# Optimization experiments

Hardware: AMD Instinct MI355X
Metric: run time of the kernel (lower is better)

Reference implementation:

```python
import jax, jax.numpy as jnp
import numpy as np

B, N, D = 4, 2048, 512
H, DA, DL = 8, 64, 64  # heads, attention_dim, linear_dim
EPS = 1e-6


def _layer_norm(x, eps=EPS):
    # F.layer_norm with no affine params
    mu = jnp.mean(x, axis=-1, keepdims=True)
    var = jnp.var(x, axis=-1, keepdims=True)
    return (x - mu) * jax.lax.rsqrt(var + eps)


def setup_inputs() -> dict:
    key = jax.random.key(0)
    k1, k2, k3, k4 = jax.random.split(key, 4)
    x = jax.random.normal(k1, (B, N, D), dtype=jnp.float32)
    # causal (lower-triangular) valid-attention mask, float {0,1}, shape (B,1,N,N)
    attention_mask = jnp.broadcast_to(
        jnp.tril(jnp.ones((N, N), dtype=jnp.float32))[None, None], (B, 1, N, N)
    )
    # _uvqk: (D, 2*H*DL + 2*H*DA), init normal(0, 0.02)
    uvqk = 0.02 * jax.random.normal(k2, (D, 2 * H * DL + 2 * H * DA), dtype=jnp.float32)
    # _o: Linear(H*DL -> D), xavier uniform
    fan_in, fan_out = H * DL, D
    limit = float(np.sqrt(6.0 / (fan_in + fan_out)))
    o_weight = jax.random.uniform(k3, (fan_out, fan_in), dtype=jnp.float32, minval=-limit, maxval=limit)
    o_bias = jnp.zeros((D,), dtype=jnp.float32)
    return {"x": x, "attention_mask": attention_mask, "uvqk": uvqk,
            "o_weight": o_weight, "o_bias": o_bias}


def reference(x, attention_mask, uvqk, o_weight, o_bias):
    b, n, _ = x.shape
    normed_x = _layer_norm(x)
    mm = jax.nn.silu(normed_x @ uvqk)  # fused uvqk projection + silu
    u, v, q, k = jnp.split(mm, [H * DL, 2 * H * DL, 2 * H * DL + H * DA], axis=-1)
    qh = q.reshape(b, n, H, DA)
    kh = k.reshape(b, n, H, DA)
    vh = v.reshape(b, n, H, DL)
    # silu-activated (non-softmax) attention with mask
    qk = jnp.einsum('bnhd,bmhd->bhnm', qh, kh)
    qk = jax.nn.silu(qk) / n
    qk = qk * attention_mask  # (B,1,N,N) broadcast over heads
    attn = jnp.einsum('bhnm,bmhd->bnhd', qk, vh).reshape(b, n, H * DL)
    # gated norm + output proj + residual
    o_input = u * _layer_norm(attn)
    return o_input @ o_weight.T + o_bias + x
```

## Files before the change

### kernel.cpp

```cpp
#include <hip/hip_runtime.h>

typedef __bf16 bf16x8 __attribute__((ext_vector_type(8)));
typedef float f32x4 __attribute__((ext_vector_type(4)));
typedef float f32x16 __attribute__((ext_vector_type(16)));

__device__ __forceinline__ unsigned short f2bf(float f) {
  return __builtin_bit_cast(unsigned short, (__bf16)f);
}
__device__ __forceinline__ float bfu2f(unsigned short b) {
  unsigned int u = ((unsigned int)b) << 16;
  return __builtin_bit_cast(float, u);
}
__device__ __forceinline__ float silu_f(float x) {
  return x * __builtin_amdgcn_rcpf(1.0f + __expf(-x));
}
__device__ __forceinline__ unsigned pk2(float a, float b) {
  return (unsigned)f2bf(a) | ((unsigned)f2bf(b) << 16);
}

template<int CPR, int NI, int SWZ>
__device__ __forceinline__ void stage16(const __bf16* __restrict__ g, int ld,
                                        __bf16* lds, int wave, int lane) {
#pragma unroll
  for (int t = 0; t < NI; ++t) {
    int cb = (wave * NI + t) * 64;
    int c = cb + lane;
    int row = c / CPR;
    int colb = (c % CPR) ^ (row & SWZ);
    __builtin_amdgcn_global_load_lds(
        (const __attribute__((address_space(1))) unsigned int*)(g + row * ld + colb * 8),
        (__attribute__((address_space(3))) unsigned int*)(lds + cb * 8),
        16, 0, 0);
  }
}


__global__ void k_tr_uvqk(const float* __restrict__ uvqk, __bf16* __restrict__ uvqkT) {
  __shared__ float tile[32][33];
  int n0 = blockIdx.x * 32, k0 = blockIdx.y * 32;
  int tx = threadIdx.x, ty = threadIdx.y;
  for (int i = ty; i < 32; i += 8)
    tile[i][tx] = uvqk[(k0 + i) * 2048 + n0 + tx];
  __syncthreads();
  for (int i = ty; i < 32; i += 8)
    uvqkT[(n0 + i) * 512 + k0 + tx] = (__bf16)tile[tx][i];
}

__global__ void k_prep(const float* __restrict__ x, __bf16* __restrict__ nx,
                       const float* __restrict__ ow, __bf16* __restrict__ owb) {
  int bid = blockIdx.x, t = threadIdx.x;
  if (bid >= 8192) {
    int i = (bid - 8192) * 128 + t;
    float4 v = ((const float4*)ow)[i];
    ushort4 o4;
    o4.x = f2bf(v.x); o4.y = f2bf(v.y); o4.z = f2bf(v.z); o4.w = f2bf(v.w);
    ((ushort4*)owb)[i] = o4;
    return;
  }
  float4 v = ((const float4*)(x + (size_t)bid * 512))[t];
  float s = v.x + v.y + v.z + v.w;
  float ss = v.x * v.x + v.y * v.y + v.z * v.z + v.w * v.w;
#pragma unroll
  for (int o = 32; o > 0; o >>= 1) { s += __shfl_down(s, o); ss += __shfl_down(ss, o); }
  __shared__ float red[4];
  if ((t & 63) == 0) { red[(t >> 6) * 2] = s; red[(t >> 6) * 2 + 1] = ss; }
  __syncthreads();
  s = red[0] + red[2]; ss = red[1] + red[3];
  float mu = s * (1.0f / 512.0f);
  float var = ss * (1.0f / 512.0f) - mu * mu;
  float rs = rsqrtf(var + 1e-6f);
  ushort4 o4;
  o4.x = f2bf((v.x - mu) * rs); o4.y = f2bf((v.y - mu) * rs);
  o4.z = f2bf((v.z - mu) * rs); o4.w = f2bf((v.w - mu) * rs);
  ((ushort4*)(nx + (size_t)bid * 512))[t] = o4;
}

__global__ __launch_bounds__(256, 3) void k_proj(
    const __bf16* __restrict__ A, const __bf16* __restrict__ Bt,
    __bf16* __restrict__ u, __bf16* __restrict__ qn,
    __bf16* __restrict__ kn, __bf16* __restrict__ vt) {
  __shared__ __bf16 As[128 * 64], Bs[128 * 64];
  int tid = threadIdx.x, wave = tid >> 6, lane = tid & 63;
  int lr = lane & 15, lq = lane >> 4;
  int bn = blockIdx.x, bm = blockIdx.y;
  const __bf16* Ag = A + (size_t)bm * 128 * 512;
  const __bf16* Bg = Bt + (size_t)bn * 128 * 512;
  int wm = (wave >> 1) * 64, wn = (wave & 1) * 64;
  f32x4 acc[4][4] = {};
  for (int k0 = 0; k0 < 512; k0 += 64) {
    stage16<8, 4, 7>(Ag + k0, 512, As, wave, lane);
    stage16<8, 4, 7>(Bg + k0, 512, Bs, wave, lane);
    __syncthreads();
#pragma unroll
    for (int kk = 0; kk < 2; ++kk) {
      int b = kk * 4 + lq;
      bf16x8 a[4], bb[4];
#pragma unroll
      for (int i = 0; i < 4; ++i) {
        int row = wm + i * 16 + lr;
        a[i] = *(const bf16x8*)(As + row * 64 + ((b ^ (row & 7)) * 8));
      }
#pragma unroll
      for (int j = 0; j < 4; ++j) {
        int row = wn + j * 16 + lr;
        bb[j] = *(const bf16x8*)(Bs + row * 64 + ((b ^ (row & 7)) * 8));
      }
#pragma unroll
      for (int i = 0; i < 4; ++i)
#pragma unroll
        for (int j = 0; j < 4; ++j)
          acc[i][j] = __builtin_amdgcn_mfma_f32_16x16x32_bf16(a[i], bb[j], acc[i][j], 0, 0, 0);
    }
    __syncthreads();
  }
  int seg = bn >> 2;
  int cb = (bn & 3) * 128 + wn;
  int rb0 = bm * 128 + wm + lq * 4;
  if (seg == 1) {
#pragma unroll
    for (int i = 0; i < 4; ++i) {
      int rb = rb0 + i * 16;
      int b = rb >> 11, n = rb & 2047;
#pragma unroll
      for (int j = 0; j < 4; ++j) {
        int c = cb + j * 16 + lr;
        ushort4 w;
        w.x = f2bf(silu_f(acc[i][j][0]) * (1.0f / 2048.0f));
        w.y = f2bf(silu_f(acc[i][j][1]) * (1.0f / 2048.0f));
        w.z = f2bf(silu_f(acc[i][j][2]) * (1.0f / 2048.0f));
        w.w = f2bf(silu_f(acc[i][j][3]) * (1.0f / 2048.0f));
        *(ushort4*)(vt + ((size_t)(b * 512 + c)) * 2048 + n) = w;
      }
    }
  } else {
    __bf16* dst = (seg == 0) ? u : ((seg == 2) ? qn : kn);
#pragma unroll
    for (int i = 0; i < 4; ++i) {
      int rb = rb0 + i * 16;
#pragma unroll
      for (int j = 0; j < 4; ++j) {
        int c = cb + j * 16 + lr;
#pragma unroll
        for (int rg = 0; rg < 4; ++rg)
          dst[(size_t)(rb + rg) * 512 + c] = (__bf16)silu_f(acc[i][j][rg]);
      }
    }
  }
}

__global__ __launch_bounds__(256, 4) void k_attn(
    const __bf16* __restrict__ qn, const __bf16* __restrict__ kn,
    const __bf16* __restrict__ vt, __bf16* __restrict__ oa,
    __bf16* __restrict__ ob) {
  __shared__ __bf16 lds[20480];
  __bf16* Qs = lds;
  __bf16* Kb0 = lds + 4096;
  __bf16* Kb1 = lds + 8192;
  __bf16* Vb0 = lds + 12288;
  __bf16* Vb1 = lds + 16384;

  int bh = blockIdx.x, p = blockIdx.y, z = blockIdx.z;
  int b = bh >> 3, hd = bh & 7;
  int tid = threadIdx.x, wave = tid >> 6, lane = tid & 63;
  int l31 = lane & 31, lh = lane >> 5;
  int wm = (wave >> 1) * 32, wn = (wave & 1) * 32;
  const __bf16* Kg = kn + (size_t)(b * 2048) * 512 + hd * 64;
  const __bf16* Vg = vt + (size_t)(b * 512 + hd * 64) * 2048;
  __bf16* Oz = z ? ob : oa;

  for (int ph = 0; ph < 2; ++ph) {
    int t = ph ? (31 - p) : p;
    int c0 = (t + 2) >> 1;
    int mlo = z ? c0 : 0;
    int cnt = (z ? (t + 1) : c0) - mlo;
    const __bf16* Qg = qn + (size_t)(b * 2048 + t * 64) * 512 + hd * 64;
    if (ph) __syncthreads();
    stage16<8, 2, 7>(Qg, 512, Qs, wave, lane);
    if (cnt > 0) {
      stage16<8, 2, 7>(Kg + (size_t)mlo * 64 * 512, 512, Kb0, wave, lane);
      stage16<8, 2, 7>(Vg + mlo * 64, 2048, Vb0, wave, lane);
    }
    __syncthreads();

    bf16x8 qf[4];
#pragma unroll
    for (int ks = 0; ks < 4; ++ks) {
      int row = wn + l31;
      qf[ks] = *(const bf16x8*)(Qs + row * 64 + (((ks * 2 + lh) ^ (row & 7)) * 8));
    }

    f32x16 po[2] = {};

    for (int i = 0; i < cnt; ++i) {
      int mt = mlo + i;
      const __bf16* Kc = (i & 1) ? Kb1 : Kb0;
      const __bf16* Vc = (i & 1) ? Vb1 : Vb0;
      if (i + 1 < cnt) {
        __bf16* Kn_ = (i & 1) ? Kb0 : Kb1;
        __bf16* Vn_ = (i & 1) ? Vb0 : Vb1;
        stage16<8, 2, 7>(Kg + (size_t)(mt + 1) * 64 * 512, 512, Kn_, wave, lane);
        stage16<8, 2, 7>(Vg + (mt + 1) * 64, 2048, Vn_, wave, lane);
      }
      f32x16 s = {};
#pragma unroll
      for (int ks = 0; ks < 4; ++ks) {
        int row = wm + l31;
        bf16x8 ak = *(const bf16x8*)(Kc + row * 64 + (((ks * 2 + lh) ^ (row & 7)) * 8));
        s = __builtin_amdgcn_mfma_f32_32x32x16_bf16(ak, qf[ks], s, 0, 0, 0);
      }
      bool diag = (mt == t);
      bool full = diag && (wm > wn + 31);
      bool dtile = diag && !full && (wm + 31 > wn);
      unsigned pk[8];
      if (full) {
#pragma unroll
        for (int q = 0; q < 8; ++q) pk[q] = 0u;
      } else {
        float vv[16];
#pragma unroll
        for (int r = 0; r < 16; ++r) {
          float xx = s[r];
          float pv = xx * __builtin_amdgcn_rcpf(1.0f + __expf(-xx));
          if (dtile) {
            int mrow = wm + 4 * lh + (r & 3) + 8 * (r >> 2);
            int ncol = wn + l31;
            if (mrow > ncol) pv = 0.0f;
          }
          vv[r] = pv;
        }
#pragma unroll
        for (int q = 0; q < 8; ++q) pk[q] = pk2(vv[2 * q], vv[2 * q + 1]);
      }
      bool lo = (lh == 0);
      unsigned xa = __shfl_xor(lo ? pk[2] : pk[0], 32);
      unsigned xb = __shfl_xor(lo ? pk[3] : pk[1], 32);
      unsigned xc = __shfl_xor(lo ? pk[6] : pk[4], 32);
      unsigned xd = __shfl_xor(lo ? pk[7] : pk[5], 32);
      union { bf16x8 v; unsigned u[4]; } f0, f1;
      f0.u[0] = lo ? pk[0] : xa;  f0.u[1] = lo ? pk[1] : xb;
      f0.u[2] = lo ? xa : pk[2];  f0.u[3] = lo ? xb : pk[3];
      f1.u[0] = lo ? pk[4] : xc;  f1.u[1] = lo ? pk[5] : xd;
      f1.u[2] = lo ? xc : pk[6];  f1.u[3] = lo ? xd : pk[7];
      bf16x8 pf[2] = { f0.v, f1.v };
#pragma unroll
      for (int t2 = 0; t2 < 2; ++t2) {
#pragma unroll
        for (int idl = 0; idl < 2; ++idl) {
          int row = idl * 32 + l31;
          bf16x8 av = *(const bf16x8*)(Vc + row * 64 +
              ((((wm >> 3) + t2 * 2 + lh) ^ (row & 7)) * 8));
          po[idl] = __builtin_amdgcn_mfma_f32_32x32x16_bf16(av, pf[t2], po[idl], 0, 0, 0);
        }
      }
      __syncthreads();
    }

    float* red = (float*)(Kb0);
    __bf16* bo = Vb1;
    if (wave >= 2) {
      float* dst = red + (wave - 2) * 2048;
#pragma unroll
      for (int idl = 0; idl < 2; ++idl)
#pragma unroll
        for (int r = 0; r < 16; ++r)
          dst[(idl * 16 + r) * 64 + lane] = po[idl][r];
    }
    __syncthreads();
    if (wave < 2) {
      float* src = red + wave * 2048;
      int nrow = wn + l31;
#pragma unroll
      for (int idl = 0; idl < 2; ++idl) {
#pragma unroll
        for (int r = 0; r < 16; ++r)
          po[idl][r] += src[(idl * 16 + r) * 64 + lane];
#pragma unroll
        for (int g = 0; g < 4; ++g) {
          int dl0 = idl * 32 + g * 8 + lh * 4;
          int addr = nrow * 64 + ((((dl0 >> 3) ^ (nrow & 7)) << 3) | (dl0 & 7));
          ushort4 w;
          w.x = f2bf(po[idl][4 * g + 0]); w.y = f2bf(po[idl][4 * g + 1]);
          w.z = f2bf(po[idl][4 * g + 2]); w.w = f2bf(po[idl][4 * g + 3]);
          *(ushort4*)(bo + addr) = w;
        }
      }
    }
    __syncthreads();
    {
      int n = tid >> 2, cc = (tid & 3) * 16;
      __bf16* gdst = Oz + (size_t)(b * 2048 + t * 64 + n) * 512 + hd * 64 + cc;
      int a0 = n * 64 + (((cc >> 3) ^ (n & 7)) << 3);
      int a1 = n * 64 + ((((cc >> 3) + 1) ^ (n & 7)) << 3);
      *(uint4*)(gdst) = *(const uint4*)(bo + a0);
      *(uint4*)(gdst + 8) = *(const uint4*)(bo + a1);
    }
  }
}

__global__ void k_oinput(const __bf16* __restrict__ oa, const __bf16* __restrict__ ob,
                         const __bf16* __restrict__ u, __bf16* __restrict__ oin) {
  int r = blockIdx.x, t = threadIdx.x;
  ushort4 a4 = ((const ushort4*)(oa + (size_t)r * 512))[t];
  ushort4 b4 = ((const ushort4*)(ob + (size_t)r * 512))[t];
  float a0 = bfu2f(a4.x) + bfu2f(b4.x), a1 = bfu2f(a4.y) + bfu2f(b4.y);
  float a2 = bfu2f(a4.z) + bfu2f(b4.z), a3 = bfu2f(a4.w) + bfu2f(b4.w);
  float s = a0 + a1 + a2 + a3;
  float ss = a0 * a0 + a1 * a1 + a2 * a2 + a3 * a3;
#pragma unroll
  for (int o = 32; o > 0; o >>= 1) { s += __shfl_down(s, o); ss += __shfl_down(ss, o); }
  __shared__ float red[4];
  if ((t & 63) == 0) { red[(t >> 6) * 2] = s; red[(t >> 6) * 2 + 1] = ss; }
  __syncthreads();
  s = red[0] + red[2]; ss = red[1] + red[3];
  float mu = s * (1.0f / 512.0f);
  float var = ss * (1.0f / 512.0f) - mu * mu;
  float rs = rsqrtf(var + 1e-6f);
  ushort4 u4 = ((const ushort4*)(u + (size_t)r * 512))[t];
  ushort4 o4;
  o4.x = f2bf(bfu2f(u4.x) * (a0 - mu) * rs);
  o4.y = f2bf(bfu2f(u4.y) * (a1 - mu) * rs);
  o4.z = f2bf(bfu2f(u4.z) * (a2 - mu) * rs);
  o4.w = f2bf(bfu2f(u4.w) * (a3 - mu) * rs);
  ((ushort4*)(oin + (size_t)r * 512))[t] = o4;
}

__global__ __launch_bounds__(256, 3) void k_out(
    const __bf16* __restrict__ A, const __bf16* __restrict__ Bt,
    const float* __restrict__ bias, const float* __restrict__ x,
    float* __restrict__ out) {
  __shared__ __bf16 As[128 * 64], Bs[128 * 64];
  int tid = threadIdx.x, wave = tid >> 6, lane = tid & 63;
  int lr = lane & 15, lq = lane >> 4;
  int bn = blockIdx.x, bm = blockIdx.y;
  const __bf16* Ag = A + (size_t)bm * 128 * 512;
  const __bf16* Bg = Bt + (size_t)bn * 128 * 512;
  int wm = (wave >> 1) * 64, wn = (wave & 1) * 64;
  f32x4 acc[4][4] = {};
  for (int k0 = 0; k0 < 512; k0 += 64) {
    stage16<8, 4, 7>(Ag + k0, 512, As, wave, lane);
    stage16<8, 4, 7>(Bg + k0, 512, Bs, wave, lane);
    __syncthreads();
#pragma unroll
    for (int kk = 0; kk < 2; ++kk) {
      int b = kk * 4 + lq;
      bf16x8 a[4], bb[4];
#pragma unroll
      for (int i = 0; i < 4; ++i) {
        int row = wm + i * 16 + lr;
        a[i] = *(const bf16x8*)(As + row * 64 + ((b ^ (row & 7)) * 8));
      }
#pragma unroll
      for (int j = 0; j < 4; ++j) {
        int row = wn + j * 16 + lr;
        bb[j] = *(const bf16x8*)(Bs + row * 64 + ((b ^ (row & 7)) * 8));
      }
#pragma unroll
      for (int i = 0; i < 4; ++i)
#pragma unroll
        for (int j = 0; j < 4; ++j)
          acc[i][j] = __builtin_amdgcn_mfma_f32_16x16x32_bf16(a[i], bb[j], acc[i][j], 0, 0, 0);
    }
    __syncthreads();
  }
  int cb = bn * 128 + wn;
  int rb0 = bm * 128 + wm + lq * 4;
#pragma unroll
  for (int j = 0; j < 4; ++j) {
    int c = cb + j * 16 + lr;
    float bv = bias[c];
#pragma unroll
    for (int i = 0; i < 4; ++i) {
      int rb = rb0 + i * 16;
#pragma unroll
      for (int rg = 0; rg < 4; ++rg) {
        size_t idx = (size_t)(rb + rg) * 512 + c;
        out[idx] = acc[i][j][rg] + bv + x[idx];
      }
    }
  }
}

extern "C" void kernel_launch(void* const* d_in, const int* in_sizes, int n_in,
                              void* d_out, int out_size, void* d_ws, size_t ws_size,
                              hipStream_t stream) {
  const float* x = (const float*)d_in[0];
  const float* uvqk = (const float*)d_in[2];
  const float* ow = (const float*)d_in[3];
  const float* obias = (const float*)d_in[4];
  float* out = (float*)d_out;

  char* w = (char*)d_ws;
  const size_t MB8 = 8u * 1024 * 1024;
  __bf16* nx    = (__bf16*)(w);
  __bf16* u     = (__bf16*)(w + MB8);
  __bf16* qn    = (__bf16*)(w + 2 * MB8);
  __bf16* kn    = (__bf16*)(w + 3 * MB8);
  __bf16* vt    = (__bf16*)(w + 4 * MB8);
  __bf16* uvqkT = (__bf16*)(w + 5 * MB8);
  __bf16* owb   = (__bf16*)(w + 5 * MB8 + 2097152);
  __bf16* Oa    = nx;
  __bf16* Ob    = (__bf16*)d_out;
  __bf16* o_in  = qn;

  k_tr_uvqk<<<dim3(64, 16), dim3(32, 8), 0, stream>>>(uvqk, uvqkT);
  k_prep<<<8704, 128, 0, stream>>>(x, nx, ow, owb);
  k_proj<<<dim3(16, 64), 256, 0, stream>>>(nx, uvqkT, u, qn, kn, vt);
  k_attn<<<dim3(32, 16, 2), 256, 0, stream>>>(qn, kn, vt, Oa, Ob);
  k_oinput<<<8192, 128, 0, stream>>>(Oa, Ob, u, o_in);
  k_out<<<dim3(4, 64), 256, 0, stream>>>(o_in, owb, obias, x, out);
}
```

Before: 210.3 us.

## Merge weight transpose into prep kernel and retile projection and output GEMMs

Folds the uvqk transpose/convert kernel into k_prep, which now processes two rows per 256-thread block, removing one launch. The projection GEMM moves to a 128x256 tile (8 MFMA columns per wave, fewer blocks, more B reuse). The output GEMM shrinks to 64x128 tiles, doubling its block count to better fill the CUs. The tradeoffs are higher register and LDS pressure in k_proj, with occupancy lowered to 2, and less A-tile reuse in k_out.

```diff
diff --git a/kernel.cpp b/kernel.cpp
--- a/kernel.cpp
+++ b/kernel.cpp
@@ -34,87 +34,92 @@
   }
 }
 
-
-__global__ void k_tr_uvqk(const float* __restrict__ uvqk, __bf16* __restrict__ uvqkT) {
-  __shared__ float tile[32][33];
-  int n0 = blockIdx.x * 32, k0 = blockIdx.y * 32;
-  int tx = threadIdx.x, ty = threadIdx.y;
-  for (int i = ty; i < 32; i += 8)
-    tile[i][tx] = uvqk[(k0 + i) * 2048 + n0 + tx];
-  __syncthreads();
-  for (int i = ty; i < 32; i += 8)
-    uvqkT[(n0 + i) * 512 + k0 + tx] = (__bf16)tile[tx][i];
-}
-
 __global__ void k_prep(const float* __restrict__ x, __bf16* __restrict__ nx,
-                       const float* __restrict__ ow, __bf16* __restrict__ owb) {
-  int bid = blockIdx.x, t = threadIdx.x;
-  if (bid >= 8192) {
-    int i = (bid - 8192) * 128 + t;
+                       const float* __restrict__ ow, __bf16* __restrict__ owb,
+                       const float* __restrict__ uvqk, __bf16* __restrict__ uvqkT) {
+  int bid = blockIdx.x, tid = threadIdx.x;
+  if (bid < 4096) {
+    int t = tid & 127;
+    int r = bid * 2 + (tid >> 7);
+    int wave = tid >> 6;
+    float4 v = ((const float4*)(x + (size_t)r * 512))[t];
+    float s = v.x + v.y + v.z + v.w;
+    float ss = v.x * v.x + v.y * v.y + v.z * v.z + v.w * v.w;
+#pragma unroll
+    for (int o = 32; o > 0; o >>= 1) { s += __shfl_down(s, o); ss += __shfl_down(ss, o); }
+    __shared__ float red[4][2];
+    if ((tid & 63) == 0) { red[wave][0] = s; red[wave][1] = ss; }
+    __syncthreads();
+    int rw = (wave >> 1) * 2;
+    s = red[rw][0] + red[rw + 1][0];
+    ss = red[rw][1] + red[rw + 1][1];
+    float mu = s * (1.0f / 512.0f);
+    float var = ss * (1.0f / 512.0f) - mu * mu;
+    float rs = rsqrtf(var + 1e-6f);
+    ushort4 o4;
+    o4.x = f2bf((v.x - mu) * rs); o4.y = f2bf((v.y - mu) * rs);
+    o4.z = f2bf((v.z - mu) * rs); o4.w = f2bf((v.w - mu) * rs);
+    ((ushort4*)(nx + (size_t)r * 512))[t] = o4;
+  } else if (bid < 4352) {
+    int i = (bid - 4096) * 256 + tid;
     float4 v = ((const float4*)ow)[i];
     ushort4 o4;
     o4.x = f2bf(v.x); o4.y = f2bf(v.y); o4.z = f2bf(v.z); o4.w = f2bf(v.w);
     ((ushort4*)owb)[i] = o4;
-    return;
-  }
-  float4 v = ((const float4*)(x + (size_t)bid * 512))[t];
-  float s = v.x + v.y + v.z + v.w;
-  float ss = v.x * v.x + v.y * v.y + v.z * v.z + v.w * v.w;
-#pragma unroll
-  for (int o = 32; o > 0; o >>= 1) { s += __shfl_down(s, o); ss += __shfl_down(ss, o); }
-  __shared__ float red[4];
-  if ((t & 63) == 0) { red[(t >> 6) * 2] = s; red[(t >> 6) * 2 + 1] = ss; }
-  __syncthreads();
-  s = red[0] + red[2]; ss = red[1] + red[3];
-  float mu = s * (1.0f / 512.0f);
-  float var = ss * (1.0f / 512.0f) - mu * mu;
-  float rs = rsqrtf(var + 1e-6f);
-  ushort4 o4;
-  o4.x = f2bf((v.x - mu) * rs); o4.y = f2bf((v.y - mu) * rs);
-  o4.z = f2bf((v.z - mu) * rs); o4.w = f2bf((v.w - mu) * rs);
-  ((ushort4*)(nx + (size_t)bid * 512))[t] = o4;
-}
-
-__global__ __launch_bounds__(256, 3) void k_proj(
+  } else {
+    __shared__ float tile[32][33];
+    int bb = bid - 4352;
+    int n0 = (bb & 63) * 32, k0 = (bb >> 6) * 32;
+    int tx = tid & 31, ty = tid >> 5;
+    for (int i = ty; i < 32; i += 8)
+      tile[i][tx] = uvqk[(k0 + i) * 2048 + n0 + tx];
+    __syncthreads();
+    for (int i = ty; i < 32; i += 8)
+      uvqkT[(n0 + i) * 512 + k0 + tx] = (__bf16)tile[tx][i];
+  }
+}
+
+__global__ __launch_bounds__(256, 2) void k_proj(
     const __bf16* __restrict__ A, const __bf16* __restrict__ Bt,
     __bf16* __restrict__ u, __bf16* __restrict__ qn,
     __bf16* __restrict__ kn, __bf16* __restrict__ vt) {
-  __shared__ __bf16 As[128 * 64], Bs[128 * 64];
+  __shared__ __bf16 As[128 * 64];
+  __shared__ __bf16 Bs[256 * 64];
   int tid = threadIdx.x, wave = tid >> 6, lane = tid & 63;
   int lr = lane & 15, lq = lane >> 4;
   int bn = blockIdx.x, bm = blockIdx.y;
   const __bf16* Ag = A + (size_t)bm * 128 * 512;
-  const __bf16* Bg = Bt + (size_t)bn * 128 * 512;
-  int wm = (wave >> 1) * 64, wn = (wave & 1) * 64;
-  f32x4 acc[4][4] = {};
+  const __bf16* Bg = Bt + (size_t)bn * 256 * 512;
+  int wm = (wave >> 1) * 64, wn2 = (wave & 1) * 128;
+  f32x4 acc[4][8] = {};
   for (int k0 = 0; k0 < 512; k0 += 64) {
     stage16<8, 4, 7>(Ag + k0, 512, As, wave, lane);
-    stage16<8, 4, 7>(Bg + k0, 512, Bs, wave, lane);
+    stage16<8, 8, 7>(Bg + k0, 512, Bs, wave, lane);
     __syncthreads();
 #pragma unroll
     for (int kk = 0; kk < 2; ++kk) {
       int b = kk * 4 + lq;
-      bf16x8 a[4], bb[4];
+      bf16x8 a[4], bb[8];
 #pragma unroll
       for (int i = 0; i < 4; ++i) {
         int row = wm + i * 16 + lr;
         a[i] = *(const bf16x8*)(As + row * 64 + ((b ^ (row & 7)) * 8));
       }
 #pragma unroll
-      for (int j = 0; j < 4; ++j) {
-        int row = wn + j * 16 + lr;
+      for (int j = 0; j < 8; ++j) {
+        int row = wn2 + j * 16 + lr;
         bb[j] = *(const bf16x8*)(Bs + row * 64 + ((b ^ (row & 7)) * 8));
       }
 #pragma unroll
       for (int i = 0; i < 4; ++i)
 #pragma unroll
-        for (int j = 0; j < 4; ++j)
+        for (int j = 0; j < 8; ++j)
           acc[i][j] = __builtin_amdgcn_mfma_f32_16x16x32_bf16(a[i], bb[j], acc[i][j], 0, 0, 0);
     }
     __syncthreads();
   }
-  int seg = bn >> 2;
-  int cb = (bn & 3) * 128 + wn;
+  int seg = bn >> 1;
+  int cb = (bn & 1) * 256 + wn2;
   int rb0 = bm * 128 + wm + lq * 4;
   if (seg == 1) {
 #pragma unroll
@@ -122,7 +127,7 @@
       int rb = rb0 + i * 16;
       int b = rb >> 11, n = rb & 2047;
 #pragma unroll
-      for (int j = 0; j < 4; ++j) {
+      for (int j = 0; j < 8; ++j) {
         int c = cb + j * 16 + lr;
         ushort4 w;
         w.x = f2bf(silu_f(acc[i][j][0]) * (1.0f / 2048.0f));
@@ -138,7 +143,7 @@
     for (int i = 0; i < 4; ++i) {
       int rb = rb0 + i * 16;
 #pragma unroll
-      for (int j = 0; j < 4; ++j) {
+      for (int j = 0; j < 8; ++j) {
         int c = cb + j * 16 + lr;
 #pragma unroll
         for (int rg = 0; rg < 4; ++rg)
@@ -324,28 +329,29 @@
   ((ushort4*)(oin + (size_t)r * 512))[t] = o4;
 }
 
-__global__ __launch_bounds__(256, 3) void k_out(
+__global__ __launch_bounds__(256, 4) void k_out(
     const __bf16* __restrict__ A, const __bf16* __restrict__ Bt,
     const float* __restrict__ bias, const float* __restrict__ x,
     float* __restrict__ out) {
-  __shared__ __bf16 As[128 * 64], Bs[128 * 64];
+  __shared__ __bf16 As[64 * 64];
+  __shared__ __bf16 Bs[128 * 64];
   int tid = threadIdx.x, wave = tid >> 6, lane = tid & 63;
   int lr = lane & 15, lq = lane >> 4;
   int bn = blockIdx.x, bm = blockIdx.y;
-  const __bf16* Ag = A + (size_t)bm * 128 * 512;
+  const __bf16* Ag = A + (size_t)bm * 64 * 512;
   const __bf16* Bg = Bt + (size_t)bn * 128 * 512;
-  int wm = (wave >> 1) * 64, wn = (wave & 1) * 64;
-  f32x4 acc[4][4] = {};
+  int wm = (wave >> 1) * 32, wn = (wave & 1) * 64;
+  f32x4 acc[2][4] = {};
   for (int k0 = 0; k0 < 512; k0 += 64) {
-    stage16<8, 4, 7>(Ag + k0, 512, As, wave, lane);
+    stage16<8, 2, 7>(Ag + k0, 512, As, wave, lane);
     stage16<8, 4, 7>(Bg + k0, 512, Bs, wave, lane);
     __syncthreads();
 #pragma unroll
     for (int kk = 0; kk < 2; ++kk) {
       int b = kk * 4 + lq;
-      bf16x8 a[4], bb[4];
-#pragma unroll
-      for (int i = 0; i < 4; ++i) {
+      bf16x8 a[2], bb[4];
+#pragma unroll
+      for (int i = 0; i < 2; ++i) {
         int row = wm + i * 16 + lr;
         a[i] = *(const bf16x8*)(As + row * 64 + ((b ^ (row & 7)) * 8));
       }
@@ -355,7 +361,7 @@
         bb[j] = *(const bf16x8*)(Bs + row * 64 + ((b ^ (row & 7)) * 8));
       }
 #pragma unroll
-      for (int i = 0; i < 4; ++i)
+      for (int i = 0; i < 2; ++i)
 #pragma unroll
         for (int j = 0; j < 4; ++j)
           acc[i][j] = __builtin_amdgcn_mfma_f32_16x16x32_bf16(a[i], bb[j], acc[i][j], 0, 0, 0);
@@ -363,13 +369,13 @@
     __syncthreads();
   }
   int cb = bn * 128 + wn;
-  int rb0 = bm * 128 + wm + lq * 4;
+  int rb0 = bm * 64 + wm + lq * 4;
 #pragma unroll
   for (int j = 0; j < 4; ++j) {
     int c = cb + j * 16 + lr;
     float bv = bias[c];
 #pragma unroll
-    for (int i = 0; i < 4; ++i) {
+    for (int i = 0; i < 2; ++i) {
       int rb = rb0 + i * 16;
 #pragma unroll
       for (int rg = 0; rg < 4; ++rg) {
@@ -402,10 +408,9 @@
   __bf16* Ob    = (__bf16*)d_out;
   __bf16* o_in  = qn;
 
-  k_tr_uvqk<<<dim3(64, 16), dim3(32, 8), 0, stream>>>(uvqk, uvqkT);
-  k_prep<<<8704, 128, 0, stream>>>(x, nx, ow, owb);
-  k_proj<<<dim3(16, 64), 256, 0, stream>>>(nx, uvqkT, u, qn, kn, vt);
+  k_prep<<<5376, 256, 0, stream>>>(x, nx, ow, owb, uvqk, uvqkT);
+  k_proj<<<dim3(8, 64), 256, 0, stream>>>(nx, uvqkT, u, qn, kn, vt);
   k_attn<<<dim3(32, 16, 2), 256, 0, stream>>>(qn, kn, vt, Oa, Ob);
   k_oinput<<<8192, 128, 0, stream>>>(Oa, Ob, u, o_in);
-  k_out<<<dim3(4, 64), 256, 0, stream>>>(o_in, owb, obias, x, out);
-}
+  k_out<<<dim3(4, 128), 256, 0, stream>>>(o_in, owb, obias, x, out);
+}
```

After: 195.7 us. 1.07x faster.
